# Kernel optimization log

Hardware: AMD Instinct MI355X
Metric: run time of the kernel (lower is better)

The kernel has to match this reference:

```python
import jax, jax.numpy as jnp
import numpy as np

D_MODEL = 1024
N_HEADS = 16
HEAD_DIM = D_MODEL // N_HEADS
D_FF = 4 * D_MODEL
LN_EPS = 1e-5  # torch nn.LayerNorm default


def setup_inputs() -> dict:
    key = jax.random.key(0)
    ks = jax.random.split(key, 6)
    B, T = 2, 2048
    s = lambda fan_in: 1.0 / np.sqrt(fan_in)
    return {
        "x": jax.random.normal(ks[0], (B, T, D_MODEL), dtype=jnp.float32),
        # weights stored as [in, out]
        "w_qkv": jax.random.normal(ks[1], (D_MODEL, 3 * D_MODEL), dtype=jnp.float32) * s(D_MODEL),
        "w_proj": jax.random.normal(ks[2], (D_MODEL, D_MODEL), dtype=jnp.float32) * s(D_MODEL),
        "ln1_g": jnp.ones((D_MODEL,), jnp.float32),
        "ln1_b": jnp.zeros((D_MODEL,), jnp.float32),
        "ln2_g": jnp.ones((D_MODEL,), jnp.float32),
        "ln2_b": jnp.zeros((D_MODEL,), jnp.float32),
        "w_ff1": jax.random.normal(ks[3], (D_MODEL, D_FF), dtype=jnp.float32) * s(D_MODEL),
        "b_ff1": jnp.zeros((D_FF,), jnp.float32),
        "w_ff2": jax.random.normal(ks[4], (D_FF, D_MODEL), dtype=jnp.float32) * s(D_FF),
        "b_ff2": jnp.zeros((D_MODEL,), jnp.float32),
    }


def _layernorm(x, g, b):
    mu = jnp.mean(x, axis=-1, keepdims=True)
    var = jnp.mean(jnp.square(x - mu), axis=-1, keepdims=True)
    return (x - mu) * jax.lax.rsqrt(var + LN_EPS) * g + b


def _attention(x, w_qkv, w_proj):
    B, T, C = x.shape
    qkv = x @ w_qkv  # [B,T,3C]
    q, k, v = jnp.split(qkv, 3, axis=-1)
    # [B, H, T, Dh]
    q = q.reshape(B, T, N_HEADS, HEAD_DIM).transpose(0, 2, 1, 3)
    k = k.reshape(B, T, N_HEADS, HEAD_DIM).transpose(0, 2, 1, 3)
    v = v.reshape(B, T, N_HEADS, HEAD_DIM).transpose(0, 2, 1, 3)
    att = jnp.einsum("bhqd,bhkd->bhqk", q, k) / np.sqrt(HEAD_DIM).astype(np.float32)
    causal = jnp.tril(jnp.ones((T, T), dtype=bool))
    att = jnp.where(causal, att, -jnp.inf)
    att = jax.nn.softmax(att, axis=-1)
    y = jnp.einsum("bhqk,bhkd->bhqd", att, v)
    y = y.transpose(0, 2, 1, 3).reshape(B, T, C)
    return y @ w_proj


def _ffn(x, w1, b1, w2, b2):
    h = jax.nn.gelu(x @ w1 + b1, approximate=False)  # torch nn.GELU default is exact
    return h @ w2 + b2


def reference(x, w_qkv, w_proj, ln1_g, ln1_b, ln2_g, ln2_b, w_ff1, b_ff1, w_ff2, b_ff2):
    x = x + _attention(_layernorm(x, ln1_g, ln1_b), w_qkv, w_proj)
    x = x + _ffn(_layernorm(x, ln2_g, ln2_b), w_ff1, b_ff1, w_ff2, b_ff2)
    return x
```

## Files before the change

### kernel.cpp

```cpp
#include <hip/hip_runtime.h>
#include <hip/hip_bf16.h>

typedef unsigned short u16;
typedef unsigned int u32;
typedef unsigned long long u64;
typedef __bf16 bf16x8 __attribute__((ext_vector_type(8)));
typedef float f32x4 __attribute__((ext_vector_type(4)));
typedef u16 u16x8 __attribute__((ext_vector_type(8)));

#define LN_EPS 1e-5f
#define SCALE_L2E 0.18033688011112042f

__device__ inline float bf2f(u16 u) { return __uint_as_float(((u32)u) << 16); }
__device__ inline u16 f2b(float f) {
    u32 u = __float_as_uint(f);
    u32 r = (u + 0x7fffu + ((u >> 16) & 1u)) >> 16;
    return (u16)r;
}
__device__ inline u32 cvtpk(float a, float b) {
    u32 r;
    asm("v_cvt_pk_bf16_f32 %0, %1, %2" : "=v"(r) : "v"(a), "v"(b));
    return r;
}

typedef __attribute__((address_space(3))) u32 as3_u32;
typedef const __attribute__((address_space(1))) u32 as1_u32;
__device__ inline void gl_lds16(const u16* g, u16* l) {
    __builtin_amdgcn_global_load_lds((as1_u32*)g, (as3_u32*)l, 16, 0, 0);
}

__device__ inline void xcd_map(int gx, int gy, int& bx, int& by) {
    int nwg = gx * gy;
    int id = blockIdx.y * gx + blockIdx.x;
    int nrc = gx >> 3;
    int cpx = nwg >> 3;
    if (((nwg | gx) & 7) == 0 && (cpx & 7) == 0 && nrc >= 1 && (8 % nrc) == 0) {
        int xcd = id & 7, loc = id >> 3, rh = cpx >> 3;
        bx = (xcd % nrc) * 8 + (loc & 7);
        by = (xcd / nrc) * rh + (loc >> 3);
    } else {
        int id2 = (nwg & 7) ? id : ((id & 7) * (nwg >> 3) + (id >> 3));
        bx = id2 % gx; by = id2 / gx;
    }
}

__global__ __launch_bounds__(256) void cast_transpose_k(const float* __restrict__ W,
                                                        u16* __restrict__ WT, int K, int N) {
    __shared__ float tile[64][65];
    int n0 = blockIdx.x * 64, k0 = blockIdx.y * 64;
    int t = threadIdx.x;
#pragma unroll
    for (int i = 0; i < 4; i++) {
        int idx = t + i * 256;
        int r = idx >> 4;
        int cq = idx & 15;
        float4 v = *reinterpret_cast<const float4*>(&W[(size_t)(k0 + r) * N + n0 + cq * 4]);
        tile[r][cq * 4 + 0] = v.x; tile[r][cq * 4 + 1] = v.y;
        tile[r][cq * 4 + 2] = v.z; tile[r][cq * 4 + 3] = v.w;
    }
    __syncthreads();
#pragma unroll
    for (int i = 0; i < 2; i++) {
        int c = t + i * 256;
        int n = c >> 3;
        int k8 = (c & 7) * 8;
        u16x8 o;
#pragma unroll
        for (int j = 0; j < 8; j++) o[j] = f2b(tile[k8 + j][n]);
        *reinterpret_cast<u16x8*>(&WT[(size_t)(n0 + n) * K + k0 + k8]) = o;
    }
}

__global__ __launch_bounds__(256) void layernorm_k(const float* __restrict__ X,
                                                   const float* __restrict__ g,
                                                   const float* __restrict__ b,
                                                   u16* __restrict__ out) {
    int row = blockIdx.x;
    int t = threadIdx.x;
    float4 v = *reinterpret_cast<const float4*>(&X[(size_t)row * 1024 + t * 4]);
    float s = v.x + v.y + v.z + v.w;
    float s2 = v.x * v.x + v.y * v.y + v.z * v.z + v.w * v.w;
#pragma unroll
    for (int o = 1; o < 64; o <<= 1) {
        s += __shfl_xor(s, o, 64);
        s2 += __shfl_xor(s2, o, 64);
    }
    __shared__ float ws[4], ws2[4];
    int wid = t >> 6, lane = t & 63;
    if (lane == 0) { ws[wid] = s; ws2[wid] = s2; }
    __syncthreads();
    float ts = ws[0] + ws[1] + ws[2] + ws[3];
    float ts2 = ws2[0] + ws2[1] + ws2[2] + ws2[3];
    float mu = ts * (1.0f / 1024.0f);
    float var = ts2 * (1.0f / 1024.0f) - mu * mu;
    float rs = rsqrtf(var + LN_EPS);
    float4 gg = *reinterpret_cast<const float4*>(&g[t * 4]);
    float4 bb = *reinterpret_cast<const float4*>(&b[t * 4]);
    u16 o4[4];
    o4[0] = f2b((v.x - mu) * rs * gg.x + bb.x);
    o4[1] = f2b((v.y - mu) * rs * gg.y + bb.y);
    o4[2] = f2b((v.z - mu) * rs * gg.z + bb.z);
    o4[3] = f2b((v.w - mu) * rs * gg.w + bb.w);
    *reinterpret_cast<ulonglong1*>(&out[(size_t)row * 1024 + t * 4]) =
        *reinterpret_cast<ulonglong1*>(o4);
}

__global__ __launch_bounds__(512, 2) void gemm256_k(const u16* __restrict__ A,
                                                    const u16* __restrict__ Bt,
                                                    int M, int N, int K,
                                                    const float* __restrict__ bias,
                                                    int do_gelu,
                                                    u16* __restrict__ outB) {
    __shared__ u16 As[2][256 * 64];
    __shared__ u16 Bs[2][256 * 64];
    int bx, by;
    xcd_map(gridDim.x, gridDim.y, bx, by);
    int m0 = by * 256, n0 = bx * 256;
    int t = threadIdx.x;
    int w = t >> 6, lane = t & 63;
    int lr = lane & 15, lg = lane >> 4;
    int wm = (w >> 2) * 128, wn = (w & 3) * 64;
    f32x4 acc[8][4] = {};

    auto stageA = [&](int buf, int kt, int h) {
        int k0 = kt * 64;
#pragma unroll
        for (int i = 0; i < 2; i++) {
            int c = t + i * 512;
            int row = h * 128 + (c >> 3), pch = c & 7;
            gl_lds16(&A[(size_t)(m0 + row) * K + k0 + ((pch ^ (row & 7)) * 8)],
                     &As[buf][h * 8192 + c * 8]);
        }
    };
    auto stageB = [&](int buf, int kt, int h) {
        int k0 = kt * 64;
#pragma unroll
        for (int i = 0; i < 2; i++) {
            int c = t + i * 512;
            int row = h * 128 + (c >> 3), pch = c & 7;
            gl_lds16(&Bt[(size_t)(n0 + row) * K + k0 + ((pch ^ (row & 7)) * 8)],
                     &Bs[buf][h * 8192 + c * 8]);
        }
    };

    int nk = K >> 6;
    stageA(0, 0, 0); stageA(0, 0, 1); stageB(0, 0, 0); stageB(0, 0, 1);
    stageB(1, 1, 0); stageB(1, 1, 1);
    asm volatile("s_waitcnt vmcnt(4)" ::: "memory");
    __builtin_amdgcn_s_barrier();
    __builtin_amdgcn_sched_barrier(0);

    for (int kt = 0; kt < nk; kt++) {
        int cur = kt & 1;
        bf16x8 af[4], bfr[4][2];
#pragma unroll
        for (int mi = 0; mi < 4; mi++) {
            int row = wm + mi * 16 + lr;
            af[mi] = *reinterpret_cast<const bf16x8*>(
                &As[cur][row * 64 + ((lg ^ (row & 7)) * 8)]);
        }
#pragma unroll
        for (int ni = 0; ni < 4; ni++) {
            int row = wn + ni * 16 + lr;
            bfr[ni][0] = *reinterpret_cast<const bf16x8*>(
                &Bs[cur][row * 64 + ((lg ^ (row & 7)) * 8)]);
            bfr[ni][1] = *reinterpret_cast<const bf16x8*>(
                &Bs[cur][row * 64 + (((4 + lg) ^ (row & 7)) * 8)]);
        }
        if (kt + 1 < nk) stageA(cur ^ 1, kt + 1, 0);
        __builtin_amdgcn_s_barrier();
        asm volatile("s_waitcnt lgkmcnt(0)" ::: "memory");
        __builtin_amdgcn_sched_barrier(0);
        __builtin_amdgcn_s_setprio(1);
#pragma unroll
        for (int mi = 0; mi < 4; mi++)
#pragma unroll
            for (int ni = 0; ni < 4; ni++)
                acc[mi][ni] = __builtin_amdgcn_mfma_f32_16x16x32_bf16(
                    af[mi], bfr[ni][0], acc[mi][ni], 0, 0, 0);
        __builtin_amdgcn_s_setprio(0);
        __builtin_amdgcn_s_barrier();
        __builtin_amdgcn_sched_barrier(0);
#pragma unroll
        for (int mi = 0; mi < 4; mi++) {
            int row = wm + mi * 16 + lr;
            af[mi] = *reinterpret_cast<const bf16x8*>(
                &As[cur][row * 64 + (((4 + lg) ^ (row & 7)) * 8)]);
        }
        if (kt + 1 < nk) stageA(cur ^ 1, kt + 1, 1);
        __builtin_amdgcn_s_barrier();
        asm volatile("s_waitcnt lgkmcnt(0)" ::: "memory");
        __builtin_amdgcn_sched_barrier(0);
        __builtin_amdgcn_s_setprio(1);
#pragma unroll
        for (int mi = 0; mi < 4; mi++)
#pragma unroll
            for (int ni = 0; ni < 4; ni++)
                acc[mi][ni] = __builtin_amdgcn_mfma_f32_16x16x32_bf16(
                    af[mi], bfr[ni][1], acc[mi][ni], 0, 0, 0);
        __builtin_amdgcn_s_setprio(0);
        __builtin_amdgcn_s_barrier();
        __builtin_amdgcn_sched_barrier(0);
#pragma unroll
        for (int mi = 0; mi < 4; mi++) {
            int row = wm + 64 + mi * 16 + lr;
            af[mi] = *reinterpret_cast<const bf16x8*>(
                &As[cur][row * 64 + ((lg ^ (row & 7)) * 8)]);
        }
        if (kt + 2 < nk) stageB(cur, kt + 2, 0);
        __builtin_amdgcn_s_barrier();
        asm volatile("s_waitcnt lgkmcnt(0)" ::: "memory");
        __builtin_amdgcn_sched_barrier(0);
        __builtin_amdgcn_s_setprio(1);
#pragma unroll
        for (int mi = 0; mi < 4; mi++)
#pragma unroll
            for (int ni = 0; ni < 4; ni++)
                acc[4 + mi][ni] = __builtin_amdgcn_mfma_f32_16x16x32_bf16(
                    af[mi], bfr[ni][0], acc[4 + mi][ni], 0, 0, 0);
        __builtin_amdgcn_s_setprio(0);
        __builtin_amdgcn_s_barrier();
        __builtin_amdgcn_sched_barrier(0);
#pragma unroll
        for (int mi = 0; mi < 4; mi++) {
            int row = wm + 64 + mi * 16 + lr;
            af[mi] = *reinterpret_cast<const bf16x8*>(
                &As[cur][row * 64 + (((4 + lg) ^ (row & 7)) * 8)]);
        }
        if (kt + 2 < nk) stageB(cur, kt + 2, 1);
        __builtin_amdgcn_s_barrier();
        asm volatile("s_waitcnt lgkmcnt(0)" ::: "memory");
        __builtin_amdgcn_sched_barrier(0);
        __builtin_amdgcn_s_setprio(1);
#pragma unroll
        for (int mi = 0; mi < 4; mi++)
#pragma unroll
            for (int ni = 0; ni < 4; ni++)
                acc[4 + mi][ni] = __builtin_amdgcn_mfma_f32_16x16x32_bf16(
                    af[mi], bfr[ni][1], acc[4 + mi][ni], 0, 0, 0);
        __builtin_amdgcn_s_setprio(0);
        asm volatile("s_waitcnt vmcnt(4)" ::: "memory");
        __builtin_amdgcn_s_barrier();
        __builtin_amdgcn_sched_barrier(0);
    }

#pragma unroll
    for (int mi = 0; mi < 8; mi++) {
#pragma unroll
        for (int ni = 0; ni < 4; ni++) {
            int col = n0 + wn + ni * 16 + lr;
#pragma unroll
            for (int i = 0; i < 4; i++) {
                int row = m0 + wm + mi * 16 + lg * 4 + i;
                float v = acc[mi][ni][i];
                if (bias) v += bias[col];
                if (do_gelu) v = 0.5f * v * (1.0f + erff(v * 0.70710678118f));
                outB[(size_t)row * N + col] = f2b(v);
            }
        }
    }
}

__global__ __launch_bounds__(256) void gemm_k(const u16* __restrict__ A,
                                              const u16* __restrict__ Bt,
                                              int M, int N, int K,
                                              const float* __restrict__ bias,
                                              const float* __restrict__ resid,
                                              int do_gelu,
                                              float* __restrict__ outF,
                                              u16* __restrict__ outB) {
    __shared__ u16 As[2][128 * 64];
    __shared__ u16 Bs[2][64 * 64];
    int bx, by;
    xcd_map(gridDim.x, gridDim.y, bx, by);
    int m0 = by * 128, n0 = bx * 64;
    int t = threadIdx.x;
    int w = t >> 6, lane = t & 63;
    int lr = lane & 15, lg = lane >> 4;
    int wm = (w >> 1) * 64, wn = (w & 1) * 32;
    f32x4 acc[4][2] = {};

    auto stage = [&](int buf, int kt) {
        int k0 = kt * 64;
#pragma unroll
        for (int i = 0; i < 4; i++) {
            int c = t + i * 256;
            int row = c >> 3, pch = c & 7;
            gl_lds16(&A[(size_t)(m0 + row) * K + k0 + ((pch ^ (row & 7)) * 8)],
                     &As[buf][c * 8]);
        }
#pragma unroll
        for (int i = 0; i < 2; i++) {
            int c = t + i * 256;
            int row = c >> 3, pch = c & 7;
            gl_lds16(&Bt[(size_t)(n0 + row) * K + k0 + ((pch ^ (row & 7)) * 8)],
                     &Bs[buf][c * 8]);
        }
    };

    int nk = K >> 6;
    stage(0, 0);
    __syncthreads();
    for (int kt = 0; kt < nk; kt++) {
        int cur = kt & 1;
        if (kt + 1 < nk) stage(cur ^ 1, kt + 1);
#pragma unroll
        for (int ks = 0; ks < 2; ks++) {
            bf16x8 af[4], bfr[2];
#pragma unroll
            for (int mi = 0; mi < 4; mi++) {
                int row = wm + mi * 16 + lr;
                af[mi] = *reinterpret_cast<const bf16x8*>(
                    &As[cur][row * 64 + (((ks * 4 + lg) ^ (row & 7)) * 8)]);
            }
#pragma unroll
            for (int ni = 0; ni < 2; ni++) {
                int row = wn + ni * 16 + lr;
                bfr[ni] = *reinterpret_cast<const bf16x8*>(
                    &Bs[cur][row * 64 + (((ks * 4 + lg) ^ (row & 7)) * 8)]);
            }
            __builtin_amdgcn_s_setprio(1);
#pragma unroll
            for (int mi = 0; mi < 4; mi++)
#pragma unroll
                for (int ni = 0; ni < 2; ni++)
                    acc[mi][ni] = __builtin_amdgcn_mfma_f32_16x16x32_bf16(
                        af[mi], bfr[ni], acc[mi][ni], 0, 0, 0);
            __builtin_amdgcn_s_setprio(0);
        }
        __syncthreads();
    }
#pragma unroll
    for (int mi = 0; mi < 4; mi++) {
#pragma unroll
        for (int ni = 0; ni < 2; ni++) {
            int col = n0 + wn + ni * 16 + lr;
#pragma unroll
            for (int i = 0; i < 4; i++) {
                int row = m0 + wm + mi * 16 + lg * 4 + i;
                float v = acc[mi][ni][i];
                if (bias) v += bias[col];
                if (do_gelu) v = 0.5f * v * (1.0f + erff(v * 0.70710678118f));
                if (resid) v += resid[(size_t)row * N + col];
                if (outF) outF[(size_t)row * N + col] = v;
                else outB[(size_t)row * N + col] = f2b(v);
            }
        }
    }
}

__global__ __launch_bounds__(256) void attn_k(const u16* __restrict__ QKV, u16* __restrict__ Y) {
    __shared__ u16 Ks[64 * 64];
    __shared__ u16 Vt[64 * 64];
    __shared__ u16 Pt[4][16 * 64];
    int u = (blockIdx.x + blockIdx.y) & 31;
    int vv = (u & 8) ? (u ^ 7) : u;
    int qt = 31 - vv;
    int bh = blockIdx.y;
    int b = bh >> 4, h = bh & 15;
    int t = threadIdx.x;
    int w = t >> 6, lane = t & 63;
    int lr = lane & 15, lg = lane >> 4;
    int q_g = qt * 64 + w * 16 + lr;
    size_t bhbase = (size_t)b * 2048 * 3072 + h * 64;

    bf16x8 qf[2];
#pragma unroll
    for (int ks = 0; ks < 2; ks++)
        qf[ks] = *reinterpret_cast<const bf16x8*>(&QKV[bhbase + (size_t)q_g * 3072 + ks * 32 + lg * 8]);

    float l = 0.0f;
    f32x4 oacc[4] = {};

    int vkey = t & 63;
    int vd0 = (t >> 6) * 8;
    int nkv = qt + 1;

    for (int kt = 0; kt < nkv; kt++) {
        size_t tb = bhbase + (size_t)(kt * 64) * 3072;
#pragma unroll
        for (int i = 0; i < 2; i++) {
            int c = t + i * 256;
            int key = c >> 3, pch = c & 7;
            gl_lds16(&QKV[tb + (size_t)key * 3072 + 1024 + ((pch ^ (key & 7)) * 8)], &Ks[c * 8]);
        }
        u16x8 vreg[2];
#pragma unroll
        for (int i = 0; i < 2; i++)
            vreg[i] = *reinterpret_cast<const u16x8*>(&QKV[tb + (size_t)vkey * 3072 + 2048 + vd0 + i * 32]);
#pragma unroll
        for (int i = 0; i < 2; i++)
#pragma unroll
            for (int j = 0; j < 8; j++) {
                int d = vd0 + i * 32 + j;
                Vt[(d * 64 + vkey) ^ ((d & 7) << 3)] = vreg[i][j];
            }
        __syncthreads();

        int kbmax = (kt == qt) ? (w + 1) : 4;
        f32x4 s[4];
        __builtin_amdgcn_s_setprio(1);
#pragma unroll
        for (int kb = 0; kb < 4; kb++) {
            if (kb < kbmax) {
                int key = kb * 16 + lr;
                bf16x8 k0 = *reinterpret_cast<const bf16x8*>(&Ks[key * 64 + ((lg ^ (key & 7)) * 8)]);
                bf16x8 k1 = *reinterpret_cast<const bf16x8*>(&Ks[key * 64 + (((4 + lg) ^ (key & 7)) * 8)]);
                f32x4 z = {0, 0, 0, 0};
                z = __builtin_amdgcn_mfma_f32_16x16x32_bf16(k0, qf[0], z, 0, 0, 0);
                s[kb] = __builtin_amdgcn_mfma_f32_16x16x32_bf16(k1, qf[1], z, 0, 0, 0);
            }
        }
        __builtin_amdgcn_s_setprio(0);

        float p[16];
        float ps4[4];
        bool diag = (kt == qt);
#pragma unroll
        for (int kb = 0; kb < 4; kb++) {
            ps4[kb] = 0.0f;
            if (kb < kbmax) {
#pragma unroll
                for (int i2 = 0; i2 < 4; i2++) {
                    float v = s[kb][i2] * SCALE_L2E;
                    if (diag && kb == w)
                        v = (kb * 16 + lg * 4 + i2 <= w * 16 + lr) ? v : -1e30f;
                    p[kb * 4 + i2] = exp2f(v);
                }
                ps4[kb] = (p[kb * 4 + 0] + p[kb * 4 + 1]) + (p[kb * 4 + 2] + p[kb * 4 + 3]);
            }
        }
        float ps = (ps4[0] + ps4[1]) + (ps4[2] + ps4[3]);
        ps += __shfl_xor(ps, 16, 64);
        ps += __shfl_xor(ps, 32, 64);
        l += ps;
#pragma unroll
        for (int kb = 0; kb < 4; kb++) {
            u32 d0 = 0, d1 = 0;
            if (kb < kbmax) {
                d0 = cvtpk(p[kb * 4 + 0], p[kb * 4 + 1]);
                d1 = cvtpk(p[kb * 4 + 2], p[kb * 4 + 3]);
            }
            int eidx = (lr * 64 + kb * 16 + lg * 4) ^ ((lr & 7) << 3);
            *reinterpret_cast<u64*>(&Pt[w][eidx]) = (u64)d0 | ((u64)d1 << 32);
        }
        __builtin_amdgcn_s_setprio(1);
#pragma unroll
        for (int ks = 0; ks < 2; ks++) {
            bf16x8 pb = *reinterpret_cast<const bf16x8*>(&Pt[w][(lr * 64 + ks * 32 + lg * 8) ^ ((lr & 7) << 3)]);
#pragma unroll
            for (int db = 0; db < 4; db++) {
                int d = db * 16 + lr;
                bf16x8 va = *reinterpret_cast<const bf16x8*>(&Vt[(d * 64 + ks * 32 + lg * 8) ^ ((d & 7) << 3)]);
                oacc[db] = __builtin_amdgcn_mfma_f32_16x16x32_bf16(va, pb, oacc[db], 0, 0, 0);
            }
        }
        __builtin_amdgcn_s_setprio(0);
        __syncthreads();
    }

    float inv = 1.0f / l;
#pragma unroll
    for (int db = 0; db < 4; db++) {
        u32 lo = cvtpk(oacc[db][0] * inv, oacc[db][1] * inv);
        u32 hi = cvtpk(oacc[db][2] * inv, oacc[db][3] * inv);
        size_t ya = (size_t)(b * 2048 + q_g) * 1024 + h * 64 + db * 16 + lg * 4;
        *reinterpret_cast<u32*>(&Y[ya]) = lo;
        *reinterpret_cast<u32*>(&Y[ya + 2]) = hi;
    }
}

extern "C" void kernel_launch(void* const* d_in, const int* in_sizes, int n_in,
                              void* d_out, int out_size, void* d_ws, size_t ws_size,
                              hipStream_t stream) {
    const float* x      = (const float*)d_in[0];
    const float* w_qkv  = (const float*)d_in[1];
    const float* w_proj = (const float*)d_in[2];
    const float* ln1_g  = (const float*)d_in[3];
    const float* ln1_b  = (const float*)d_in[4];
    const float* ln2_g  = (const float*)d_in[5];
    const float* ln2_b  = (const float*)d_in[6];
    const float* w_ff1  = (const float*)d_in[7];
    const float* b_ff1  = (const float*)d_in[8];
    const float* w_ff2  = (const float*)d_in[9];
    const float* b_ff2  = (const float*)d_in[10];
    float* out = (float*)d_out;

    char* ws = (char*)d_ws;
    u16* qkv    = (u16*)(ws);
    u16* act16  = (u16*)(ws + 25165824);
    float* x2   = (float*)(ws + 33554432);
    u16* hbuf   = (u16*)(ws + 50331648);
    u16* wqkvT  = (u16*)(ws + 83886080);
    u16* wprojT = (u16*)(ws + 90177536);
    u16* wff1T  = (u16*)(ws + 92274688);
    u16* wff2T  = (u16*)(ws + 100663296);

    cast_transpose_k<<<dim3(48, 16), 256, 0, stream>>>(w_qkv, wqkvT, 1024, 3072);
    cast_transpose_k<<<dim3(16, 16), 256, 0, stream>>>(w_proj, wprojT, 1024, 1024);
    cast_transpose_k<<<dim3(64, 16), 256, 0, stream>>>(w_ff1, wff1T, 1024, 4096);
    cast_transpose_k<<<dim3(16, 64), 256, 0, stream>>>(w_ff2, wff2T, 4096, 1024);

    layernorm_k<<<4096, 256, 0, stream>>>(x, ln1_g, ln1_b, act16);
    gemm256_k<<<dim3(12, 16), 512, 0, stream>>>(act16, wqkvT, 4096, 3072, 1024,
                                                nullptr, 0, qkv);
    attn_k<<<dim3(32, 32), 256, 0, stream>>>(qkv, act16);
    gemm_k<<<dim3(16, 32), 256, 0, stream>>>(act16, wprojT, 4096, 1024, 1024,
                                             nullptr, x, 0, x2, nullptr);
    layernorm_k<<<4096, 256, 0, stream>>>(x2, ln2_g, ln2_b, act16);
    gemm256_k<<<dim3(16, 16), 512, 0, stream>>>(act16, wff1T, 4096, 4096, 1024,
                                                b_ff1, 1, hbuf);
    gemm_k<<<dim3(16, 32), 256, 0, stream>>>(hbuf, wff2T, 4096, 1024, 4096,
                                             b_ff2, x2, 0, out, nullptr);
}
```

Baseline: 298.6 us.

## Double attention query tile to 128 rows with 8 waves per block

The attention kernel now processes 128 query rows per block using 512 threads (8 waves) instead of 64 rows with 256 threads. Each K/V tile loaded into shared memory is then reused by twice as many query rows, which halves global K/V traffic and the number of staging passes. Causal masking is generalised to per-wave diagonal block detection. In exchange there are half as many blocks, waves that are fully masked idle on the diagonal tiles, and larger blocks limit occupancy.

```diff
diff --git a/kernel.cpp b/kernel.cpp
--- a/kernel.cpp
+++ b/kernel.cpp
@@ -349,19 +349,20 @@
     }
 }
 
-__global__ __launch_bounds__(256) void attn_k(const u16* __restrict__ QKV, u16* __restrict__ Y) {
+__global__ __launch_bounds__(512) void attn_k(const u16* __restrict__ QKV, u16* __restrict__ Y) {
     __shared__ u16 Ks[64 * 64];
     __shared__ u16 Vt[64 * 64];
-    __shared__ u16 Pt[4][16 * 64];
-    int u = (blockIdx.x + blockIdx.y) & 31;
+    __shared__ u16 Pt[8][16 * 64];
+    int u = (blockIdx.x + blockIdx.y) & 15;
     int vv = (u & 8) ? (u ^ 7) : u;
-    int qt = 31 - vv;
+    int qt = 15 - vv;
     int bh = blockIdx.y;
     int b = bh >> 4, h = bh & 15;
     int t = threadIdx.x;
     int w = t >> 6, lane = t & 63;
     int lr = lane & 15, lg = lane >> 4;
-    int q_g = qt * 64 + w * 16 + lr;
+    int q_g = qt * 128 + w * 16 + lr;
+    int qw = qt * 8 + w;
     size_t bhbase = (size_t)b * 2048 * 3072 + h * 64;
 
     bf16x8 qf[2];
@@ -374,30 +375,24 @@
 
     int vkey = t & 63;
     int vd0 = (t >> 6) * 8;
-    int nkv = qt + 1;
+    int nkv = 2 * qt + 2;
 
     for (int kt = 0; kt < nkv; kt++) {
         size_t tb = bhbase + (size_t)(kt * 64) * 3072;
-#pragma unroll
-        for (int i = 0; i < 2; i++) {
-            int c = t + i * 256;
-            int key = c >> 3, pch = c & 7;
-            gl_lds16(&QKV[tb + (size_t)key * 3072 + 1024 + ((pch ^ (key & 7)) * 8)], &Ks[c * 8]);
-        }
-        u16x8 vreg[2];
-#pragma unroll
-        for (int i = 0; i < 2; i++)
-            vreg[i] = *reinterpret_cast<const u16x8*>(&QKV[tb + (size_t)vkey * 3072 + 2048 + vd0 + i * 32]);
-#pragma unroll
-        for (int i = 0; i < 2; i++)
-#pragma unroll
-            for (int j = 0; j < 8; j++) {
-                int d = vd0 + i * 32 + j;
-                Vt[(d * 64 + vkey) ^ ((d & 7) << 3)] = vreg[i][j];
-            }
+        {
+            int key = t >> 3, pch = t & 7;
+            gl_lds16(&QKV[tb + (size_t)key * 3072 + 1024 + ((pch ^ (key & 7)) * 8)], &Ks[t * 8]);
+        }
+        u16x8 vreg = *reinterpret_cast<const u16x8*>(&QKV[tb + (size_t)vkey * 3072 + 2048 + vd0]);
+#pragma unroll
+        for (int j = 0; j < 8; j++) {
+            int d = vd0 + j;
+            Vt[(d * 64 + vkey) ^ ((d & 7) << 3)] = vreg[j];
+        }
         __syncthreads();
 
-        int kbmax = (kt == qt) ? (w + 1) : 4;
+        int kbm = qw - kt * 4 + 1;
+        int kbmax = kbm < 0 ? 0 : (kbm > 4 ? 4 : kbm);
         f32x4 s[4];
         __builtin_amdgcn_s_setprio(1);
 #pragma unroll
@@ -415,16 +410,16 @@
 
         float p[16];
         float ps4[4];
-        bool diag = (kt == qt);
 #pragma unroll
         for (int kb = 0; kb < 4; kb++) {
             ps4[kb] = 0.0f;
             if (kb < kbmax) {
+                bool diag = (kt * 4 + kb == qw);
 #pragma unroll
                 for (int i2 = 0; i2 < 4; i2++) {
                     float v = s[kb][i2] * SCALE_L2E;
-                    if (diag && kb == w)
-                        v = (kb * 16 + lg * 4 + i2 <= w * 16 + lr) ? v : -1e30f;
+                    if (diag)
+                        v = (lg * 4 + i2 <= lr) ? v : -1e30f;
                     p[kb * 4 + i2] = exp2f(v);
                 }
                 ps4[kb] = (p[kb * 4 + 0] + p[kb * 4 + 1]) + (p[kb * 4 + 2] + p[kb * 4 + 3]);
@@ -504,7 +499,7 @@
     layernorm_k<<<4096, 256, 0, stream>>>(x, ln1_g, ln1_b, act16);
     gemm256_k<<<dim3(12, 16), 512, 0, stream>>>(act16, wqkvT, 4096, 3072, 1024,
                                                 nullptr, 0, qkv);
-    attn_k<<<dim3(32, 32), 256, 0, stream>>>(qkv, act16);
+    attn_k<<<dim3(16, 32), 512, 0, stream>>>(qkv, act16);
     gemm_k<<<dim3(16, 32), 256, 0, stream>>>(act16, wprojT, 4096, 1024, 1024,
                                              nullptr, x, 0, x2, nullptr);
     layernorm_k<<<4096, 256, 0, stream>>>(x2, ln2_g, ln2_b, act16);
```

Measured after the change: 310.8 us. +4.1%, slower.
